# Performance work log

Hardware: AMD Instinct MI355X
Metric: run time of the kernel (lower is better)

Reference implementation:

```python
import jax, jax.numpy as jnp
import numpy as np

H = W = 128
R = 2
H2, W2 = H // R, W // R
TOPK = 3
NSEG = H * W + 1  # segment 0 = background


def _ccl(binary):
    """8-connected component labeling via iterative max-label propagation.
    binary: [H,W] bool. Returns int32 labels, 0 = background; each component
    gets a unique (arbitrary) positive id = max pixel index in the component."""
    idx = jnp.arange(1, H * W + 1, dtype=jnp.int32).reshape(H, W)
    lab0 = jnp.where(binary, idx, 0)

    def cond(c):
        return c[1]

    def body(c):
        lab, _ = c
        nb = jax.lax.reduce_window(lab, jnp.int32(0), jax.lax.max,
                                   (3, 3), (1, 1), 'SAME')  # 3x3 incl. self
        new = jnp.where(binary, nb, 0)
        return new, jnp.any(new != lab)

    lab, _ = jax.lax.while_loop(cond, body, (lab0, jnp.bool_(True)))
    return lab


def _process_one(prob_i, feat_i):
    """prob_i: [1,H,W], feat_i: [Cf,H,W] -> [3*Cf, H2, W2]."""
    p = prob_i[0]
    binary = p > 0.5
    lab = _ccl(binary).reshape(-1)  # [H*W] segment ids

    ones = jnp.ones((H * W,), jnp.float32)
    count = jax.ops.segment_sum(ones, lab, num_segments=NSEG)
    conf_sum = jax.ops.segment_sum(p.reshape(-1), lab, num_segments=NSEG)
    mean_conf = conf_sum / jnp.maximum(count, 1.0)

    rows = jnp.repeat(jnp.arange(H, dtype=jnp.int32), W)
    cols = jnp.tile(jnp.arange(W, dtype=jnp.int32), H)
    min_r = jax.ops.segment_min(rows, lab, num_segments=NSEG)
    max_r = jax.ops.segment_max(rows, lab, num_segments=NSEG)
    min_c = jax.ops.segment_min(cols, lab, num_segments=NSEG)
    max_c = jax.ops.segment_max(cols, lab, num_segments=NSEG)

    valid = (count > 0) & (jnp.arange(NSEG) > 0)
    score = jnp.where(valid, mean_conf, -jnp.inf)
    _, top_idx = jax.lax.top_k(score, TOPK)  # regions sorted by mean confidence
    K = jnp.sum(valid.astype(jnp.int32))     # number of connected regions

    # duplication rules: K==0 -> full image x3; K==1 -> [f0,f0,f0];
    # K==2 -> [f0,f0,f1]; K>=3 -> [f0,f1,f2]
    i0, i1 = top_idx[0], top_idx[1]
    slots = jnp.where(K >= 3, top_idx,
            jnp.where(K == 2, jnp.stack([i0, i0, i1]),
                      jnp.stack([i0, i0, i0])))

    mr = jnp.where(K > 0, min_r[slots], 0)
    Mr = jnp.where(K > 0, max_r[slots] + 1, H)  # bbox half-open, regionprops style
    mc = jnp.where(K > 0, min_c[slots], 0)
    Mc = jnp.where(K > 0, max_c[slots] + 1, W)

    def crop(a, b, c, d):
        # PyTorch nearest interpolate: src = floor(dst * in/out)
        r = a + (jnp.arange(H2) * (b - a)) // H2
        cc = c + (jnp.arange(W2) * (d - c)) // W2
        return feat_i[:, r][:, :, cc]  # [Cf, H2, W2]

    out = jax.vmap(crop)(mr, Mr, mc, Mc)  # [3, Cf, H2, W2]
    return out.reshape(-1, H2, W2)         # [3*Cf, H2, W2]


def setup_inputs() -> dict:
    key = jax.random.key(0)
    k1, k2 = jax.random.split(key)
    prob = jax.random.uniform(k1, (16, 1, H, W), dtype=jnp.float32)
    feat = jax.random.normal(k2, (16, 192, H, W), dtype=jnp.float32)
    return {"prob": prob, "feat": feat}


def reference(prob, feat):
    return jax.vmap(_process_one)(prob, feat)  # [B, 3*Cf, H2, W2]
```

## Files before the change

### kernel.cpp

```cpp
#include <hip/hip_runtime.h>
#include <limits.h>

#define HH 128
#define WW_ 128
#define HW 16384
#define NB 16
#define CF 192
#define H2 64
#define W2 64
#define NRUN 8192
#define NCOMP 4096

typedef float vf4 __attribute__((ext_vector_type(4)));
typedef unsigned long long ull;


__device__ inline int uf_find(int* par, int x) {
    volatile int* vp = (volatile int*)par;
    int p = vp[x];
    while (p != x) {
        int g = vp[p];
        vp[x] = g;
        x = g;
        p = vp[x];
    }
    return x;
}

__device__ inline void uf_union(int* par, int a, int b) {
    int ra = uf_find(par, a);
    int rb = uf_find(par, b);
    while (ra != rb) {
        if (ra < rb) { int t = ra; ra = rb; rb = t; }
        int old = atomicCAS(&par[ra], ra, rb);
        if (old == ra) return;
        ra = uf_find(par, old);
        rb = uf_find(par, rb);
    }
}


__device__ inline int getbit2(ull lo, ull hi, int c) {
    return (int)(((c < 64) ? (lo >> c) : (hi >> (c - 64))) & 1ULL);
}

__device__ inline int leading_ones(ull v) {
    ull nv = ~v;
    return (nv == 0ULL) ? 64 : __clzll(nv);
}

__device__ inline int trailing_ones(ull v) {
    ull nv = ~v;
    return (nv == 0ULL) ? 64 : (__ffsll(nv) - 1);
}

__device__ inline int run_start_col(ull lo, ull hi, int c) {
    if (c < 64) {
        int ones = leading_ones(lo << (63 - c));
        return c - ones + 1;
    }
    int ones = leading_ones(hi << (127 - c));
    int rs = c - ones + 1;
    if (rs == 64) rs -= leading_ones(lo);
    return rs;
}

__device__ inline int run_end_col(ull lo, ull hi, int c) {
    if (c >= 64) {
        return c + trailing_ones(hi >> (c - 64)) - 1;
    }
    int e = c + trailing_ones(lo >> c) - 1;
    if (e == 63) e += trailing_ones(hi);
    return e;
}

__device__ inline int run_index(ull rs_lo, ull rs_hi, int cs) {
    if (cs < 64)  return __popcll(rs_lo & ((1ULL << cs) - 1ULL));
    if (cs == 64) return __popcll(rs_lo);
    return __popcll(rs_lo) + __popcll(rs_hi & ((1ULL << (cs - 64)) - 1ULL));
}

__device__ inline void top3_ins(float s, int id, int x,
    float& s0, float& s1, float& s2,
    int& i0, int& i1, int& i2,
    int& x0, int& x1, int& x2)
{
    if (x < 0) return;
    if (s > s0 || (s == s0 && id < i0)) {
        s2 = s1; i2 = i1; x2 = x1;
        s1 = s0; i1 = i0; x1 = x0;
        s0 = s;  i0 = id; x0 = x;
    } else if (s > s1 || (s == s1 && id < i1)) {
        s2 = s1; i2 = i1; x2 = x1;
        s1 = s;  i1 = id; x1 = x;
    } else if (s > s2 || (s == s2 && id < i2)) {
        s2 = s;  i2 = id; x2 = x;
    }
}


__global__ __launch_bounds__(1024) void ccl_kernel(
    const float* __restrict__ prob, int* __restrict__ bbox)
{
    __shared__ int parent[NRUN];
    __shared__ ull rowmask[HH][2];
    __shared__ int   lcnt[NCOMP];
    __shared__ float lconf[NCOMP];
    __shared__ int lminr[NCOMP], lmaxr[NCOMP];
    __shared__ int lminc[NCOMP], lmaxc[NCOMP];
    __shared__ int lmaxid[NCOMP];
    __shared__ int snroots;
    __shared__ float wss[48];
    __shared__ int wid_[48], wrx[48];

    const int b = blockIdx.x;
    const int tid = threadIdx.x;
    const float* p = prob + (size_t)b * HW;

    if (tid == 0) snroots = 0;

    #pragma unroll
    for (int k = 0; k < HW / 1024; ++k) {
        int i = k * 1024 + tid;
        ull m = __ballot(p[i] > 0.5f);
        if ((tid & 63) == 0) rowmask[i >> 7][(i >> 6) & 1] = m;
    }
    for (int j = tid; j < NCOMP; j += 1024) {
        lcnt[j] = 0; lconf[j] = 0.f;
        lminr[j] = INT_MAX; lmaxr[j] = -1;
        lminc[j] = INT_MAX; lmaxc[j] = -1;
        lmaxid[j] = 0;
    }
    __syncthreads();

    for (int rid = tid; rid < NRUN; rid += 1024) {
        int r = rid >> 6;
        ull lo = rowmask[r][0], hi = rowmask[r][1];
        ull rs_lo = lo & ~(lo << 1);
        ull rs_hi = hi & ~((hi << 1) | (lo >> 63));
        int nruns = __popcll(rs_lo) + __popcll(rs_hi);
        if ((rid & 63) < nruns) parent[rid] = rid;
    }
    __syncthreads();

    for (int k = 0; k < HW / 1024; ++k) {
        int i = k * 1024 + tid;
        int r = i >> 7, c = i & 127;
        if (r == 0) continue;
        ull lo = rowmask[r][0], hi = rowmask[r][1];
        if (!getbit2(lo, hi, c)) continue;
        ull ulo = rowmask[r - 1][0], uhi = rowmask[r - 1][1];
        int l  = (c > 0)   ? getbit2(lo, hi, c - 1) : 0;
        int rt = (c < 127) ? getbit2(lo, hi, c + 1) : 0;
        int up = getbit2(ulo, uhi, c);
        int ul = (c > 0)   ? getbit2(ulo, uhi, c - 1) : 0;
        int ur = (c < 127) ? getbit2(ulo, uhi, c + 1) : 0;
        bool u1 = up && !(l && ul);
        bool u2 = !up && ul && !l;
        bool u3 = !up && ur && !rt;
        if (!(u1 | u2 | u3)) continue;
        ull rs_lo = lo & ~(lo << 1),   rs_hi = hi & ~((hi << 1) | (lo >> 63));
        ull urs_lo = ulo & ~(ulo << 1), urs_hi = uhi & ~((uhi << 1) | (ulo >> 63));
        int cs = run_start_col(lo, hi, c);
        int rid = (r << 6) + run_index(rs_lo, rs_hi, cs);
        int ub = (r - 1) << 6;
        if (u1) uf_union(parent, rid, ub + run_index(urs_lo, urs_hi, run_start_col(ulo, uhi, c)));
        if (u2) uf_union(parent, rid, ub + run_index(urs_lo, urs_hi, run_start_col(ulo, uhi, c - 1)));
        if (u3) uf_union(parent, rid, ub + run_index(urs_lo, urs_hi, run_start_col(ulo, uhi, c + 1)));
    }
    __syncthreads();

    for (int rid = tid; rid < NRUN; rid += 1024) {
        int r = rid >> 6;
        ull lo = rowmask[r][0], hi = rowmask[r][1];
        ull rs_lo = lo & ~(lo << 1);
        ull rs_hi = hi & ~((hi << 1) | (lo >> 63));
        int nruns = __popcll(rs_lo) + __popcll(rs_hi);
        if ((rid & 63) < nruns) parent[rid] = uf_find(parent, rid);
    }
    __syncthreads();
    for (int rid = tid; rid < NRUN; rid += 1024) {
        int r = rid >> 6;
        ull lo = rowmask[r][0], hi = rowmask[r][1];
        ull rs_lo = lo & ~(lo << 1);
        ull rs_hi = hi & ~((hi << 1) | (lo >> 63));
        int nruns = __popcll(rs_lo) + __popcll(rs_hi);
        if ((rid & 63) < nruns && parent[rid] == rid) {
            int idx = atomicAdd(&snroots, 1);
            parent[rid] = NRUN + idx;
        }
    }
    __syncthreads();

    {
        int row = tid >> 3;
        int w0 = (tid & 7) * 16;
        ull lo = rowmask[row][0], hi = rowmask[row][1];
        ull rs_lo = lo & ~(lo << 1);
        ull rs_hi = hi & ~((hi << 1) | (lo >> 63));
        ull seg = ((w0 < 64) ? (rs_lo >> w0) : (rs_hi >> (w0 - 64))) & 0xFFFFULL;
        int curIdx = -1, aCnt = 0, aMinc = 0, aMaxc = 0, aMaxid = 0;
        float aConf = 0.f;
        while (seg) {
            int c = w0 + (__ffsll(seg) - 1);
            seg &= seg - 1;
            int e = run_end_col(lo, hi, c);
            int rid = (row << 6) + run_index(rs_lo, rs_hi, c);
            int v = parent[rid];
            int idx = (v >= NRUN) ? (v - NRUN) : (parent[v] - NRUN);
            float s = 0.f;
            for (int j = c; j <= e; ++j) s += p[(row << 7) + j];
            if (idx == curIdx) {
                aCnt += e - c + 1; aConf += s;
                aMaxc = e; aMaxid = (row << 7) + e + 1;
            } else {
                if (curIdx >= 0) {
                    atomicAdd(&lcnt[curIdx], aCnt);
                    atomicAdd(&lconf[curIdx], aConf);
                    atomicMin(&lminr[curIdx], row);
                    atomicMax(&lmaxr[curIdx], row);
                    atomicMin(&lminc[curIdx], aMinc);
                    atomicMax(&lmaxc[curIdx], aMaxc);
                    atomicMax(&lmaxid[curIdx], aMaxid);
                }
                curIdx = idx; aCnt = e - c + 1; aConf = s;
                aMinc = c; aMaxc = e; aMaxid = (row << 7) + e + 1;
            }
        }
        if (curIdx >= 0) {
            atomicAdd(&lcnt[curIdx], aCnt);
            atomicAdd(&lconf[curIdx], aConf);
            atomicMin(&lminr[curIdx], row);
            atomicMax(&lmaxr[curIdx], row);
            atomicMin(&lminc[curIdx], aMinc);
            atomicMax(&lmaxc[curIdx], aMaxc);
            atomicMax(&lmaxid[curIdx], aMaxid);
        }
    }
    __syncthreads();

    const int n = snroots;
    float s0 = -INFINITY, s1 = -INFINITY, s2 = -INFINITY;
    int i0 = INT_MAX, i1 = INT_MAX, i2 = INT_MAX;
    int x0 = -1, x1 = -1, x2 = -1;
    for (int j = tid; j < n; j += 1024) {
        float s = lconf[j] / (float)lcnt[j];
        top3_ins(s, lmaxid[j], j, s0, s1, s2, i0, i1, i2, x0, x1, x2);
    }
    for (int off = 32; off; off >>= 1) {
        float bs0 = __shfl_xor(s0, off), bs1 = __shfl_xor(s1, off), bs2 = __shfl_xor(s2, off);
        int bi0 = __shfl_xor(i0, off), bi1 = __shfl_xor(i1, off), bi2 = __shfl_xor(i2, off);
        int bx0 = __shfl_xor(x0, off), bx1 = __shfl_xor(x1, off), bx2 = __shfl_xor(x2, off);
        top3_ins(bs0, bi0, bx0, s0, s1, s2, i0, i1, i2, x0, x1, x2);
        top3_ins(bs1, bi1, bx1, s0, s1, s2, i0, i1, i2, x0, x1, x2);
        top3_ins(bs2, bi2, bx2, s0, s1, s2, i0, i1, i2, x0, x1, x2);
    }
    if ((tid & 63) == 0) {
        int w = tid >> 6;
        wss[w * 3 + 0] = s0; wid_[w * 3 + 0] = i0; wrx[w * 3 + 0] = x0;
        wss[w * 3 + 1] = s1; wid_[w * 3 + 1] = i1; wrx[w * 3 + 1] = x1;
        wss[w * 3 + 2] = s2; wid_[w * 3 + 2] = i2; wrx[w * 3 + 2] = x2;
    }
    __syncthreads();

    if (tid == 0) {
        float t0 = -INFINITY, t1 = -INFINITY, t2 = -INFINITY;
        int ti0 = INT_MAX, ti1 = INT_MAX, ti2 = INT_MAX;
        int tx0 = -1, tx1 = -1, tx2 = -1;
        for (int t = 0; t < 48; ++t)
            top3_ins(wss[t], wid_[t], wrx[t], t0, t1, t2, ti0, ti1, ti2, tx0, tx1, tx2);
        int K = n;
        int roots[3];
        if (K >= 3)      { roots[0] = tx0; roots[1] = tx1; roots[2] = tx2; }
        else if (K == 2) { roots[0] = tx0; roots[1] = tx0; roots[2] = tx1; }
        else             { roots[0] = tx0; roots[1] = tx0; roots[2] = tx0; }
        for (int slot = 0; slot < 3; ++slot) {
            int mr, h, mc, w;
            if (K == 0) { mr = 0; h = HH; mc = 0; w = WW_; }
            else {
                int rt = roots[slot];
                mr = lminr[rt]; h = lmaxr[rt] + 1 - mr;
                mc = lminc[rt]; w = lmaxc[rt] + 1 - mc;
            }
            int* o = bbox + (b * 3 + slot) * 4;
            o[0] = mr; o[1] = h; o[2] = mc; o[3] = w;
        }
    }
}


__global__ __launch_bounds__(256) void crop_kernel(
    const float* __restrict__ feat, const int* __restrict__ bbox,
    float* __restrict__ out)
{
    const int gid = blockIdx.x * 256 + threadIdx.x;
    const int x4 = gid & 15;
    const int y  = (gid >> 4) & 63;
    const int t  = gid >> 10;
    const int c  = t % CF;
    const int bs = t / CF;
    const int* bb = bbox + bs * 4;
    const int mr = bb[0], h = bb[1], mc = bb[2], w = bb[3];
    const int r = mr + ((y * h) >> 6);
    const int bimg = bs / 3;
    const float* row = feat + (((size_t)bimg * CF + c) * HH + r) * WW_;
    const int x = x4 * 4;
    vf4 v;
    v.x = row[mc + (((x + 0) * w) >> 6)];
    v.y = row[mc + (((x + 1) * w) >> 6)];
    v.z = row[mc + (((x + 2) * w) >> 6)];
    v.w = row[mc + (((x + 3) * w) >> 6)];
    __builtin_nontemporal_store(v, (vf4*)out + gid);
}


extern "C" void kernel_launch(void* const* d_in, const int* in_sizes, int n_in,
                              void* d_out, int out_size, void* d_ws, size_t ws_size,
                              hipStream_t stream) {
    const float* prob = (const float*)d_in[0];
    const float* feat = (const float*)d_in[1];
    float* out = (float*)d_out;

    int* bbox = (int*)d_ws;

    hipLaunchKernelGGL(ccl_kernel, dim3(NB), dim3(1024), 0, stream,
                       prob, bbox);
    const int total4 = NB * 3 * CF * H2 * (W2 / 4);
    hipLaunchKernelGGL(crop_kernel, dim3(total4 / 256), dim3(256), 0, stream,
                       feat, bbox, out);
}
```

Before: 386.4 us.

## Split per-image CCL into stripe-local labeling plus cross-stripe merge kernel

Replaces the single 16-block CCL kernel with 128 stripe blocks (8 stripes of 16 rows per image) that label and reduce their components locally, writing per-component stats and boundary-row run labels to workspace. A second per-image kernel unions components across stripe boundaries, folds their stats, and does the top-3 selection. Stats accumulation now uses the vector-loaded probability values per thread instead of re-reading global memory per run. The aim is to spread the serial CCL phase over more CUs; the cost is an extra launch and a global-memory round trip for per-stripe stats.

```diff
diff --git a/kernel.cpp b/kernel.cpp
--- a/kernel.cpp
+++ b/kernel.cpp
@@ -8,8 +8,13 @@
 #define CF 192
 #define H2 64
 #define W2 64
-#define NRUN 8192
-#define NCOMP 4096
+
+#define SH 16
+#define NSPI 8
+#define NST 128
+#define SC 512
+#define NCI 4096
+#define NLRUN 1024
 
 typedef float vf4 __attribute__((ext_vector_type(4)));
 typedef unsigned long long ull;
@@ -63,15 +68,6 @@
     int rs = c - ones + 1;
     if (rs == 64) rs -= leading_ones(lo);
     return rs;
-}
-
-__device__ inline int run_end_col(ull lo, ull hi, int c) {
-    if (c >= 64) {
-        return c + trailing_ones(hi >> (c - 64)) - 1;
-    }
-    int e = c + trailing_ones(lo >> c) - 1;
-    if (e == 63) e += trailing_ones(hi);
-    return e;
 }
 
 __device__ inline int run_index(ull rs_lo, ull rs_hi, int cs) {
@@ -99,43 +95,59 @@
 }
 
 
-__global__ __launch_bounds__(1024) void ccl_kernel(
-    const float* __restrict__ prob, int* __restrict__ bbox)
+__global__ __launch_bounds__(256) void stripe_ccl(
+    const float* __restrict__ prob,
+    int* __restrict__ nlocg, int* __restrict__ gcnt, float* __restrict__ gconf,
+    int* __restrict__ gminr, int* __restrict__ gmaxr,
+    int* __restrict__ gminc, int* __restrict__ gmaxc,
+    int* __restrict__ gmaxid, int* __restrict__ brun, ull* __restrict__ bmask)
 {
-    __shared__ int parent[NRUN];
-    __shared__ ull rowmask[HH][2];
-    __shared__ int   lcnt[NCOMP];
-    __shared__ float lconf[NCOMP];
-    __shared__ int lminr[NCOMP], lmaxr[NCOMP];
-    __shared__ int lminc[NCOMP], lmaxc[NCOMP];
-    __shared__ int lmaxid[NCOMP];
-    __shared__ int snroots;
-    __shared__ float wss[48];
-    __shared__ int wid_[48], wrx[48];
-
-    const int b = blockIdx.x;
+    __shared__ ull rowm[SH][2];
+    __shared__ unsigned char m8[256];
+    __shared__ int parent[NLRUN];
+    __shared__ int   lcnt[SC];
+    __shared__ float lconf[SC];
+    __shared__ int lminr[SC], lmaxr[SC], lminc[SC], lmaxc[SC], lmaxid[SC];
+    __shared__ int snloc;
+
+    const int g = blockIdx.x;
+    const int b = g >> 3, s = g & 7;
+    const int row0 = s * SH;
     const int tid = threadIdx.x;
-    const float* p = prob + (size_t)b * HW;
-
-    if (tid == 0) snroots = 0;
-
-    #pragma unroll
-    for (int k = 0; k < HW / 1024; ++k) {
-        int i = k * 1024 + tid;
-        ull m = __ballot(p[i] > 0.5f);
-        if ((tid & 63) == 0) rowmask[i >> 7][(i >> 6) & 1] = m;
-    }
-    for (int j = tid; j < NCOMP; j += 1024) {
+    const int row = tid >> 4;
+    const int w0 = (tid & 15) * 8;
+
+    if (tid == 0) snloc = 0;
+
+    const float* p = prob + (size_t)b * HW + (size_t)((row0 + row) << 7) + w0;
+    vf4 va = *(const vf4*)p;
+    vf4 vb = *(const vf4*)(p + 4);
+    int mask8 = 0;
+    mask8 |= (va.x > 0.5f) << 0; mask8 |= (va.y > 0.5f) << 1;
+    mask8 |= (va.z > 0.5f) << 2; mask8 |= (va.w > 0.5f) << 3;
+    mask8 |= (vb.x > 0.5f) << 4; mask8 |= (vb.y > 0.5f) << 5;
+    mask8 |= (vb.z > 0.5f) << 6; mask8 |= (vb.w > 0.5f) << 7;
+    m8[tid] = (unsigned char)mask8;
+    for (int j = tid; j < SC; j += 256) {
         lcnt[j] = 0; lconf[j] = 0.f;
         lminr[j] = INT_MAX; lmaxr[j] = -1;
         lminc[j] = INT_MAX; lmaxc[j] = -1;
         lmaxid[j] = 0;
     }
     __syncthreads();
-
-    for (int rid = tid; rid < NRUN; rid += 1024) {
+    if (tid < 32) {
+        int r = tid >> 1, half = tid & 1;
+        ull v = 0;
+        #pragma unroll
+        for (int k2 = 0; k2 < 8; ++k2)
+            v |= (ull)m8[(r << 4) + (half << 3) + k2] << (k2 * 8);
+        rowm[r][half] = v;
+    }
+    __syncthreads();
+
+    for (int rid = tid; rid < NLRUN; rid += 256) {
         int r = rid >> 6;
-        ull lo = rowmask[r][0], hi = rowmask[r][1];
+        ull lo = rowm[r][0], hi = rowm[r][1];
         ull rs_lo = lo & ~(lo << 1);
         ull rs_hi = hi & ~((hi << 1) | (lo >> 63));
         int nruns = __popcll(rs_lo) + __popcll(rs_hi);
@@ -143,13 +155,11 @@
     }
     __syncthreads();
 
-    for (int k = 0; k < HW / 1024; ++k) {
-        int i = k * 1024 + tid;
-        int r = i >> 7, c = i & 127;
-        if (r == 0) continue;
-        ull lo = rowmask[r][0], hi = rowmask[r][1];
+    for (int i = tid; i < (SH - 1) * 128; i += 256) {
+        int r = 1 + (i >> 7), c = i & 127;
+        ull lo = rowm[r][0], hi = rowm[r][1];
         if (!getbit2(lo, hi, c)) continue;
-        ull ulo = rowmask[r - 1][0], uhi = rowmask[r - 1][1];
+        ull ulo = rowm[r - 1][0], uhi = rowm[r - 1][1];
         int l  = (c > 0)   ? getbit2(lo, hi, c - 1) : 0;
         int rt = (c < 127) ? getbit2(lo, hi, c + 1) : 0;
         int up = getbit2(ulo, uhi, c);
@@ -170,68 +180,71 @@
     }
     __syncthreads();
 
-    for (int rid = tid; rid < NRUN; rid += 1024) {
+    for (int rid = tid; rid < NLRUN; rid += 256) {
         int r = rid >> 6;
-        ull lo = rowmask[r][0], hi = rowmask[r][1];
+        ull lo = rowm[r][0], hi = rowm[r][1];
         ull rs_lo = lo & ~(lo << 1);
         ull rs_hi = hi & ~((hi << 1) | (lo >> 63));
         int nruns = __popcll(rs_lo) + __popcll(rs_hi);
         if ((rid & 63) < nruns) parent[rid] = uf_find(parent, rid);
     }
     __syncthreads();
-    for (int rid = tid; rid < NRUN; rid += 1024) {
+    for (int rid = tid; rid < NLRUN; rid += 256) {
         int r = rid >> 6;
-        ull lo = rowmask[r][0], hi = rowmask[r][1];
+        ull lo = rowm[r][0], hi = rowm[r][1];
         ull rs_lo = lo & ~(lo << 1);
         ull rs_hi = hi & ~((hi << 1) | (lo >> 63));
         int nruns = __popcll(rs_lo) + __popcll(rs_hi);
         if ((rid & 63) < nruns && parent[rid] == rid) {
-            int idx = atomicAdd(&snroots, 1);
-            parent[rid] = NRUN + idx;
+            int idx = atomicAdd(&snloc, 1);
+            parent[rid] = NLRUN + idx;
         }
     }
     __syncthreads();
 
     {
-        int row = tid >> 3;
-        int w0 = (tid & 7) * 16;
-        ull lo = rowmask[row][0], hi = rowmask[row][1];
+        ull lo = rowm[row][0], hi = rowm[row][1];
         ull rs_lo = lo & ~(lo << 1);
         ull rs_hi = hi & ~((hi << 1) | (lo >> 63));
-        ull seg = ((w0 < 64) ? (rs_lo >> w0) : (rs_hi >> (w0 - 64))) & 0xFFFFULL;
+        const float vv[8] = {va.x, va.y, va.z, va.w, vb.x, vb.y, vb.z, vb.w};
+        const int imr = row0 + row;
         int curIdx = -1, aCnt = 0, aMinc = 0, aMaxc = 0, aMaxid = 0;
         float aConf = 0.f;
-        while (seg) {
-            int c = w0 + (__ffsll(seg) - 1);
-            seg &= seg - 1;
-            int e = run_end_col(lo, hi, c);
-            int rid = (row << 6) + run_index(rs_lo, rs_hi, c);
-            int v = parent[rid];
-            int idx = (v >= NRUN) ? (v - NRUN) : (parent[v] - NRUN);
-            float s = 0.f;
-            for (int j = c; j <= e; ++j) s += p[(row << 7) + j];
-            if (idx == curIdx) {
-                aCnt += e - c + 1; aConf += s;
-                aMaxc = e; aMaxid = (row << 7) + e + 1;
-            } else {
-                if (curIdx >= 0) {
-                    atomicAdd(&lcnt[curIdx], aCnt);
-                    atomicAdd(&lconf[curIdx], aConf);
-                    atomicMin(&lminr[curIdx], row);
-                    atomicMax(&lmaxr[curIdx], row);
-                    atomicMin(&lminc[curIdx], aMinc);
-                    atomicMax(&lmaxc[curIdx], aMaxc);
-                    atomicMax(&lmaxid[curIdx], aMaxid);
+        bool prevfg = false;
+        #pragma unroll
+        for (int j = 0; j < 8; ++j) {
+            bool fg = (mask8 >> j) & 1;
+            if (fg) {
+                int c = w0 + j;
+                if (!prevfg) {
+                    int cs = run_start_col(lo, hi, c);
+                    int rid = (row << 6) + run_index(rs_lo, rs_hi, cs);
+                    int v = parent[rid];
+                    int idx = (v >= NLRUN) ? v - NLRUN : parent[v] - NLRUN;
+                    if (idx != curIdx) {
+                        if (curIdx >= 0) {
+                            atomicAdd(&lcnt[curIdx], aCnt);
+                            atomicAdd(&lconf[curIdx], aConf);
+                            atomicMin(&lminr[curIdx], imr);
+                            atomicMax(&lmaxr[curIdx], imr);
+                            atomicMin(&lminc[curIdx], aMinc);
+                            atomicMax(&lmaxc[curIdx], aMaxc);
+                            atomicMax(&lmaxid[curIdx], aMaxid);
+                        }
+                        curIdx = idx; aCnt = 0; aConf = 0.f;
+                        aMinc = c; aMaxc = c; aMaxid = 0;
+                    }
                 }
-                curIdx = idx; aCnt = e - c + 1; aConf = s;
-                aMinc = c; aMaxc = e; aMaxid = (row << 7) + e + 1;
+                aCnt++; aConf += vv[j]; aMaxc = c;
+                aMaxid = (imr << 7) + c + 1;
             }
+            prevfg = fg;
         }
         if (curIdx >= 0) {
             atomicAdd(&lcnt[curIdx], aCnt);
             atomicAdd(&lconf[curIdx], aConf);
-            atomicMin(&lminr[curIdx], row);
-            atomicMax(&lmaxr[curIdx], row);
+            atomicMin(&lminr[curIdx], imr);
+            atomicMax(&lmaxr[curIdx], imr);
             atomicMin(&lminc[curIdx], aMinc);
             atomicMax(&lmaxc[curIdx], aMaxc);
             atomicMax(&lmaxid[curIdx], aMaxid);
@@ -239,14 +252,123 @@
     }
     __syncthreads();
 
-    const int n = snroots;
+    const int nl = snloc;
+    for (int j = tid; j < nl; j += 256) {
+        int d = (g << 9) + j;
+        gcnt[d] = lcnt[j];  gconf[d] = lconf[j];
+        gminr[d] = lminr[j]; gmaxr[d] = lmaxr[j];
+        gminc[d] = lminc[j]; gmaxc[d] = lmaxc[j];
+        gmaxid[d] = lmaxid[j];
+    }
+    if (tid == 0) nlocg[g] = nl;
+    if (tid < 128) {
+        int br = tid >> 6;
+        int j = tid & 63;
+        int r = br ? (SH - 1) : 0;
+        ull lo = rowm[r][0], hi = rowm[r][1];
+        ull rs_lo = lo & ~(lo << 1);
+        ull rs_hi = hi & ~((hi << 1) | (lo >> 63));
+        int nruns = __popcll(rs_lo) + __popcll(rs_hi);
+        if (j < nruns) {
+            int rid = (r << 6) + j;
+            int v = parent[rid];
+            brun[(g << 7) + (br << 6) + j] = (v >= NLRUN) ? v - NLRUN : parent[v] - NLRUN;
+        }
+        if (j == 0) {
+            bmask[(g << 2) + (br << 1) + 0] = lo;
+            bmask[(g << 2) + (br << 1) + 1] = hi;
+        }
+    }
+}
+
+
+__global__ __launch_bounds__(1024) void merge_kernel(
+    const int* __restrict__ nlocg, const int* __restrict__ gcnt,
+    const float* __restrict__ gconf,
+    const int* __restrict__ gminr, const int* __restrict__ gmaxr,
+    const int* __restrict__ gminc, const int* __restrict__ gmaxc,
+    const int* __restrict__ gmaxid, const int* __restrict__ brun,
+    const ull* __restrict__ bmask, int* __restrict__ bbox)
+{
+    __shared__ int parent2[NCI];
+    __shared__ int   cnt2[NCI];
+    __shared__ float conf2[NCI];
+    __shared__ int minr2[NCI], maxr2[NCI], minc2[NCI], maxc2[NCI], maxid2[NCI];
+    __shared__ int sK;
+    __shared__ float wss[48];
+    __shared__ int wid_[48], wrx[48];
+
+    const int b = blockIdx.x;
+    const int tid = threadIdx.x;
+    if (tid == 0) sK = 0;
+    for (int i = tid; i < NCI; i += 1024) { parent2[i] = i; cnt2[i] = 0; }
+    __syncthreads();
+
+    for (int s = 0; s < NSPI; ++s) {
+        int g = (b << 3) + s;
+        int n = nlocg[g];
+        for (int j = tid; j < n; j += 1024) {
+            int d = (s << 9) + j, e = (g << 9) + j;
+            cnt2[d] = gcnt[e];  conf2[d] = gconf[e];
+            minr2[d] = gminr[e]; maxr2[d] = gmaxr[e];
+            minc2[d] = gminc[e]; maxc2[d] = gmaxc[e];
+            maxid2[d] = gmaxid[e];
+        }
+    }
+    __syncthreads();
+
+    for (int i = tid; i < 7 * 128; i += 1024) {
+        int k = 1 + (i >> 7), c = i & 127;
+        int gLo = (b << 3) + k, gUp = gLo - 1;
+        ull lo = bmask[(gLo << 2) + 0], hi = bmask[(gLo << 2) + 1];
+        if (!getbit2(lo, hi, c)) continue;
+        ull ulo = bmask[(gUp << 2) + 2], uhi = bmask[(gUp << 2) + 3];
+        int l  = (c > 0)   ? getbit2(lo, hi, c - 1) : 0;
+        int rt = (c < 127) ? getbit2(lo, hi, c + 1) : 0;
+        int up = getbit2(ulo, uhi, c);
+        int ul = (c > 0)   ? getbit2(ulo, uhi, c - 1) : 0;
+        int ur = (c < 127) ? getbit2(ulo, uhi, c + 1) : 0;
+        bool u1 = up && !(l && ul);
+        bool u2 = !up && ul && !l;
+        bool u3 = !up && ur && !rt;
+        if (!(u1 | u2 | u3)) continue;
+        ull rs_lo = lo & ~(lo << 1),   rs_hi = hi & ~((hi << 1) | (lo >> 63));
+        ull urs_lo = ulo & ~(ulo << 1), urs_hi = uhi & ~((uhi << 1) | (ulo >> 63));
+        int cs = run_start_col(lo, hi, c);
+        int myid = (k << 9) + brun[(gLo << 7) + run_index(rs_lo, rs_hi, cs)];
+        int ubase = (k - 1) << 9;
+        if (u1) uf_union(parent2, myid, ubase + brun[(gUp << 7) + 64 + run_index(urs_lo, urs_hi, run_start_col(ulo, uhi, c))]);
+        if (u2) uf_union(parent2, myid, ubase + brun[(gUp << 7) + 64 + run_index(urs_lo, urs_hi, run_start_col(ulo, uhi, c - 1))]);
+        if (u3) uf_union(parent2, myid, ubase + brun[(gUp << 7) + 64 + run_index(urs_lo, urs_hi, run_start_col(ulo, uhi, c + 1))]);
+    }
+    __syncthreads();
+
+    for (int i = tid; i < NCI; i += 1024) {
+        if (cnt2[i] > 0) {
+            int r = uf_find(parent2, i);
+            if (r != i) {
+                atomicAdd(&cnt2[r], cnt2[i]);   atomicAdd(&conf2[r], conf2[i]);
+                atomicMin(&minr2[r], minr2[i]); atomicMax(&maxr2[r], maxr2[i]);
+                atomicMin(&minc2[r], minc2[i]); atomicMax(&maxc2[r], maxc2[i]);
+                atomicMax(&maxid2[r], maxid2[i]);
+            }
+        }
+    }
+    __syncthreads();
+
     float s0 = -INFINITY, s1 = -INFINITY, s2 = -INFINITY;
     int i0 = INT_MAX, i1 = INT_MAX, i2 = INT_MAX;
     int x0 = -1, x1 = -1, x2 = -1;
-    for (int j = tid; j < n; j += 1024) {
-        float s = lconf[j] / (float)lcnt[j];
-        top3_ins(s, lmaxid[j], j, s0, s1, s2, i0, i1, i2, x0, x1, x2);
-    }
+    int kc = 0;
+    for (int i = tid; i < NCI; i += 1024) {
+        if (parent2[i] == i && cnt2[i] > 0) {
+            ++kc;
+            float sc = conf2[i] / (float)cnt2[i];
+            top3_ins(sc, maxid2[i], i, s0, s1, s2, i0, i1, i2, x0, x1, x2);
+        }
+    }
+    for (int off = 32; off; off >>= 1) kc += __shfl_xor(kc, off);
+    if ((tid & 63) == 0) atomicAdd(&sK, kc);
     for (int off = 32; off; off >>= 1) {
         float bs0 = __shfl_xor(s0, off), bs1 = __shfl_xor(s1, off), bs2 = __shfl_xor(s2, off);
         int bi0 = __shfl_xor(i0, off), bi1 = __shfl_xor(i1, off), bi2 = __shfl_xor(i2, off);
@@ -269,7 +391,7 @@
         int tx0 = -1, tx1 = -1, tx2 = -1;
         for (int t = 0; t < 48; ++t)
             top3_ins(wss[t], wid_[t], wrx[t], t0, t1, t2, ti0, ti1, ti2, tx0, tx1, tx2);
-        int K = n;
+        int K = sK;
         int roots[3];
         if (K >= 3)      { roots[0] = tx0; roots[1] = tx1; roots[2] = tx2; }
         else if (K == 2) { roots[0] = tx0; roots[1] = tx0; roots[2] = tx1; }
@@ -279,8 +401,8 @@
             if (K == 0) { mr = 0; h = HH; mc = 0; w = WW_; }
             else {
                 int rt = roots[slot];
-                mr = lminr[rt]; h = lmaxr[rt] + 1 - mr;
-                mc = lminc[rt]; w = lmaxc[rt] + 1 - mc;
+                mr = minr2[rt]; h = maxr2[rt] + 1 - mr;
+                mc = minc2[rt]; w = maxc2[rt] + 1 - mc;
             }
             int* o = bbox + (b * 3 + slot) * 4;
             o[0] = mr; o[1] = h; o[2] = mc; o[3] = w;
@@ -321,10 +443,25 @@
     const float* feat = (const float*)d_in[1];
     float* out = (float*)d_out;
 
-    int* bbox = (int*)d_ws;
-
-    hipLaunchKernelGGL(ccl_kernel, dim3(NB), dim3(1024), 0, stream,
-                       prob, bbox);
+    int* ws = (int*)d_ws;
+    int* bbox   = ws;
+    int* nlocg  = ws + 192;
+    int* gcnt   = ws + 320;
+    float* gconf = (float*)(ws + 320 + 1 * 65536);
+    int* gminr  = ws + 320 + 2 * 65536;
+    int* gmaxr  = ws + 320 + 3 * 65536;
+    int* gminc  = ws + 320 + 4 * 65536;
+    int* gmaxc  = ws + 320 + 5 * 65536;
+    int* gmaxid = ws + 320 + 6 * 65536;
+    int* brun   = ws + 320 + 7 * 65536;
+    ull* bmask  = (ull*)(ws + 320 + 7 * 65536 + 16384);
+
+    hipLaunchKernelGGL(stripe_ccl, dim3(NST), dim3(256), 0, stream,
+                       prob, nlocg, gcnt, gconf, gminr, gmaxr, gminc, gmaxc,
+                       gmaxid, brun, bmask);
+    hipLaunchKernelGGL(merge_kernel, dim3(NB), dim3(1024), 0, stream,
+                       nlocg, gcnt, gconf, gminr, gmaxr, gminc, gmaxc,
+                       gmaxid, brun, bmask, bbox);
     const int total4 = NB * 3 * CF * H2 * (W2 / 4);
     hipLaunchKernelGGL(crop_kernel, dim3(total4 / 256), dim3(256), 0, stream,
                        feat, bbox, out);
```

Result: faster. 351.7 us (-9.0%).
